# Kernel tuning notes

Measured on AMD Instinct MI355X. Metric: run time of the kernel, lower is better.

Reference implementation:

```python
import jax, jax.numpy as jnp
import numpy as np

NUM_CODES = 512
CODE_DIM = 64
BATCH = 1048576


def setup_inputs() -> dict:
    key = jax.random.key(0)
    k1, k2 = jax.random.split(key)
    z_e = jax.random.normal(k1, (BATCH, CODE_DIM), dtype=jnp.float32)
    bound = 1.0 / np.sqrt(float(CODE_DIM))
    codebook = jax.random.uniform(
        k2, (NUM_CODES, CODE_DIM), dtype=jnp.float32, minval=-bound, maxval=bound
    )
    return {"z_e": z_e, "codebook": codebook}


def reference(z_e, codebook):
    # ||z_e||^2 - 2 z_e . e_j + ||e_j||^2  -> (batch, num_codes)
    distances = (
        jnp.sum(z_e**2, axis=1, keepdims=True)
        - 2.0 * (z_e @ codebook.T)
        + jnp.sum(codebook**2, axis=1)
    )
    indices = jnp.argmin(distances, axis=1)          # (batch,)
    z_q = codebook[indices]                           # gather (batch, code_dim)
    # straight-through estimator
    z_q_st = z_e + jax.lax.stop_gradient(z_q - z_e)
    commitment_loss = jnp.mean((jax.lax.stop_gradient(z_e) - z_q) ** 2)
    return (z_q_st, indices, commitment_loss)
```

## Files before the change

### kernel.cpp

```cpp
#include <hip/hip_runtime.h>
#include <stdint.h>


#define DIM 64
#define NCODE 512
#define RPB 128
#define MARGIN 2e-3f
#define BIAS 64.0f
#define ZEXB 8
#define WS_NEED (NCODE * DIM * 2 * sizeof(unsigned short) + NCODE * sizeof(float))

typedef __attribute__((ext_vector_type(8))) short short8;
typedef __attribute__((ext_vector_type(4))) float f32x4;
typedef unsigned long long ull;

__device__ __forceinline__ float bf2f(unsigned short u) {
    union { unsigned u; float f; } c; c.u = ((unsigned)u) << 16; return c.f;
}
__device__ __forceinline__ unsigned short f2bf(float f) {
    union { float f; unsigned u; } c; c.f = f;
    unsigned r = c.u + 0x7fffu + ((c.u >> 16) & 1u);
    return (unsigned short)(r >> 16);
}
__device__ __forceinline__ unsigned fkey(float v) {
    union { float f; unsigned u; } c; c.f = v;
    return c.u ^ ((unsigned)((int)c.u >> 31) | 0x80000000u);
}

__device__ __forceinline__ float np_sumsq64_sse(const float* x) {
    #pragma clang fp contract(off)
    float T[4];
    #pragma unroll
    for (int l = 0; l < 4; ++l) {
        float A[8];
        #pragma unroll
        for (int j = 0; j < 8; ++j) {
            float u = x[4 * j + l];
            float v = x[32 + 4 * j + l];
            A[j] = u * u + v * v;
        }
        T[l] = ((A[0] + A[1]) + (A[2] + A[3])) + ((A[4] + A[5]) + (A[6] + A[7]));
    }
    return (T[0] + T[1]) + (T[2] + T[3]);
}

__global__ void vq_zero_loss(float* __restrict__ out, long long lidx) {
    if (threadIdx.x == 0) out[lidx] = 0.f;
}

__global__ __launch_bounds__(NCODE) void vq_prep(
    const float* __restrict__ cb, unsigned short* __restrict__ ws)
{
    const int code = threadIdx.x;
    unsigned short* cbhi = ws;
    unsigned short* cblo = ws + NCODE * DIM;
    float* ce2g = (float*)(ws + 2 * NCODE * DIM);

    float sp[4];
    #pragma unroll
    for (int cl = 0; cl < 4; ++cl) {
        float s = 0.f;
        #pragma unroll
        for (int ks = 0; ks < 2; ++ks) {
            #pragma unroll
            for (int t = 0; t < 8; ++t) {
                int k = ks * 32 + cl * 8 + t;
                float v = cb[code * DIM + k];
                unsigned short hb = f2bf(v);
                cbhi[code * DIM + k] = hb;
                cblo[code * DIM + k] = f2bf(v - bf2f(hb));
                s = fmaf(v, v, s);
            }
        }
        sp[cl] = s;
    }
    ce2g[code] = ((sp[0] + sp[1]) + (sp[2] + sp[3])) + BIAS;
}

template <bool PRE>
__global__ __launch_bounds__(512, 4) void vq_main(
    const float* __restrict__ z, const float* __restrict__ cb,
    float* __restrict__ out, const unsigned short* __restrict__ ws,
    long long batch)
{
    __shared__ __align__(16) unsigned short zhi[RPB * DIM];
    __shared__ __align__(16) unsigned short zlo[RPB * DIM];
    __shared__ float zsq[RPB];
    __shared__ float arrB[RPB][9];
    __shared__ float arrB2[RPB][9];
    __shared__ unsigned arrI[RPB][9];
    __shared__ ull cpack[RPB];
    __shared__ unsigned ck2[RPB];
    __shared__ float wsum[8];
    __shared__ int s_flag[RPB];
    __shared__ int s_nflag;
    __shared__ float s_zex[ZEXB][DIM];
    __shared__ ull s_win[ZEXB];

    const int tid = threadIdx.x, lane = tid & 63, wid = tid >> 6;
    const long long R0 = (long long)blockIdx.x * RPB;
    short8* zhi8 = (short8*)zhi;
    short8* zlo8 = (short8*)zlo;

    if (tid == 0) s_nflag = 0;

    #pragma unroll
    for (int p = 0; p < 2; ++p) {
        int L = p * 512 + tid;
        int row = L >> 3, c = L & 7;
        const float4* g = (const float4*)(z + (R0 + row) * DIM + c * 8);
        float4 f0 = g[0], f1 = g[1];
        float v[8] = {f0.x, f0.y, f0.z, f0.w, f1.x, f1.y, f1.z, f1.w};
        short8 h, l;
        float s = 0.f;
        #pragma unroll
        for (int t = 0; t < 8; ++t) {
            unsigned short hb = f2bf(v[t]);
            h[t] = (short)hb;
            l[t] = (short)f2bf(v[t] - bf2f(hb));
            s = fmaf(v[t], v[t], s);
        }
        s += __shfl_xor(s, 1);
        s += __shfl_xor(s, 2);
        s += __shfl_xor(s, 4);
        if ((tid & 7) == 0) zsq[row] = s;
        int slot = row * 8 + (c ^ (row & 7));
        zhi8[slot] = h;
        zlo8[slot] = l;
    }

    short8 bhi[4][2], blo[4][2];
    float ce2[4];
    if constexpr (PRE) {
        const unsigned short* cbhi = ws;
        const unsigned short* cblo = ws + NCODE * DIM;
        const float* ce2g = (const float*)(ws + 2 * NCODE * DIM);
        #pragma unroll
        for (int ct = 0; ct < 4; ++ct) {
            int code = wid * 64 + ct * 16 + (lane & 15);
            #pragma unroll
            for (int ks = 0; ks < 2; ++ks) {
                int k = ks * 32 + (lane >> 4) * 8;
                bhi[ct][ks] = *(const short8*)(cbhi + code * DIM + k);
                blo[ct][ks] = *(const short8*)(cblo + code * DIM + k);
            }
            ce2[ct] = ce2g[code];
        }
    } else {
        #pragma unroll
        for (int ct = 0; ct < 4; ++ct) {
            int code = wid * 64 + ct * 16 + (lane & 15);
            float s = 0.f;
            #pragma unroll
            for (int ks = 0; ks < 2; ++ks) {
                int k = ks * 32 + (lane >> 4) * 8;
                const float4* g = (const float4*)(cb + code * DIM + k);
                float4 f0 = g[0], f1 = g[1];
                float v[8] = {f0.x, f0.y, f0.z, f0.w, f1.x, f1.y, f1.z, f1.w};
                short8 h, l;
                #pragma unroll
                for (int t = 0; t < 8; ++t) {
                    unsigned short hb = f2bf(v[t]);
                    h[t] = (short)hb;
                    l[t] = (short)f2bf(v[t] - bf2f(hb));
                    s = fmaf(v[t], v[t], s);
                }
                bhi[ct][ks] = h;
                blo[ct][ks] = l;
            }
            s += __shfl_xor(s, 16);
            s += __shfl_xor(s, 32);
            ce2[ct] = s + BIAS;
        }
    }

    __syncthreads();

    for (int rt = 0; rt < 8; ++rt) {
        int arow = rt * 16 + (lane & 15);
        int swz = arow & 7;
        int c0 = (lane >> 4) ^ swz, c1 = (4 + (lane >> 4)) ^ swz;
        short8 ah0 = zhi8[arow * 8 + c0], ah1 = zhi8[arow * 8 + c1];
        short8 al0 = zlo8[arow * 8 + c0], al1 = zlo8[arow * 8 + c1];

        float b1[4] = {3.4e38f, 3.4e38f, 3.4e38f, 3.4e38f};
        float b2[4] = {3.4e38f, 3.4e38f, 3.4e38f, 3.4e38f};
        unsigned bi[4] = {0, 0, 0, 0};

        #pragma unroll
        for (int ct = 0; ct < 4; ++ct) {
            f32x4 a = {0.f, 0.f, 0.f, 0.f};
            a = __builtin_amdgcn_mfma_f32_16x16x32_bf16(ah0, bhi[ct][0], a, 0, 0, 0);
            a = __builtin_amdgcn_mfma_f32_16x16x32_bf16(ah1, bhi[ct][1], a, 0, 0, 0);
            a = __builtin_amdgcn_mfma_f32_16x16x32_bf16(ah0, blo[ct][0], a, 0, 0, 0);
            a = __builtin_amdgcn_mfma_f32_16x16x32_bf16(ah1, blo[ct][1], a, 0, 0, 0);
            a = __builtin_amdgcn_mfma_f32_16x16x32_bf16(al0, bhi[ct][0], a, 0, 0, 0);
            a = __builtin_amdgcn_mfma_f32_16x16x32_bf16(al1, bhi[ct][1], a, 0, 0, 0);
            #pragma unroll
            for (int r = 0; r < 4; ++r) {
                float v = fmaf(-2.f, a[r], ce2[ct]);
                unsigned idx = (unsigned)(wid * 64 + ct * 16 + (lane & 15));
                float nb2 = __builtin_amdgcn_fmed3f(v, b1[r], b2[r]);
                bi[r] = (v < b1[r]) ? idx : bi[r];
                b1[r] = fminf(v, b1[r]);
                b2[r] = nb2;
            }
        }

        #pragma unroll
        for (int r = 0; r < 4; ++r) {
            float x1 = b1[r], x2 = b2[r];
            unsigned xi = bi[r];
            #pragma unroll
            for (int m = 1; m <= 8; m <<= 1) {
                float ob  = __shfl_xor(x1, m);
                float ob2 = __shfl_xor(x2, m);
                unsigned oi = __shfl_xor(xi, m);
                float mx = fmaxf(x1, ob);
                x2 = fminf(fminf(x2, ob2), mx);
                xi = (ob < x1) ? oi : xi;
                x1 = fminf(x1, ob);
            }
            if ((lane & 15) == 0) {
                int row = rt * 16 + (lane >> 4) * 4 + r;
                arrB[row][wid]  = x1;
                arrB2[row][wid] = x2;
                arrI[row][wid]  = xi;
            }
        }
    }
    __syncthreads();

    if (tid < 128) {
        int row = tid;
        float b1 = arrB[row][0], b2 = arrB2[row][0];
        unsigned bi = arrI[row][0];
        #pragma unroll
        for (int w = 1; w < 8; ++w) {
            float ob = arrB[row][w];
            float ob2 = arrB2[row][w];
            unsigned oi = arrI[row][w];
            float mx = fmaxf(b1, ob);
            b2 = fminf(fminf(b2, ob2), mx);
            bi = (ob < b1) ? oi : bi;
            b1 = fminf(b1, ob);
        }
        cpack[row] = ((ull)__float_as_uint(b1) << 32) | bi;
        ck2[row] = __float_as_uint(b2);
    }
    __syncthreads();

    {
        int row = tid >> 2, j = tid & 3;
        ull best = cpack[row];
        unsigned bk2 = ck2[row];
        unsigned code = (unsigned)best;
        long long grow = R0 + row;

        float4* out4 = (float4*)out;
        const float4* cb4 = (const float4*)cb;
        #pragma unroll
        for (int t = 0; t < 4; ++t)
            out4[grow * 16 + j * 4 + t] = cb4[(long long)code * 16 + j * 4 + t];

        float d = 0.f;
        if (j == 0) {
            out[batch * DIM + grow] = (float)code;
            float v1b = __uint_as_float((unsigned)(best >> 32));
            float v2b = __uint_as_float(bk2);
            d = zsq[row] + (v1b - BIAS);
            if (v2b - v1b < MARGIN) {
                int p = atomicAdd(&s_nflag, 1);
                s_flag[p] = row;
            }
        }
        #pragma unroll
        for (int m = 1; m < 64; m <<= 1) d += __shfl_xor(d, m);
        if (lane == 0) wsum[wid] = d;
    }
    __syncthreads();
    if (tid == 0) {
        float s = 0.f;
        #pragma unroll
        for (int w = 0; w < 8; ++w) s += wsum[w];
        atomicAdd(&out[batch * DIM + batch], s * (1.0f / 67108864.0f));
    }

    int nf = s_nflag;
    if (nf > 0) {
        float ce[64];
        const float4* cb4 = (const float4*)cb;
        #pragma unroll
        for (int q = 0; q < 16; ++q) {
            float4 v = cb4[tid * 16 + q];
            ce[q * 4 + 0] = v.x; ce[q * 4 + 1] = v.y;
            ce[q * 4 + 2] = v.z; ce[q * 4 + 3] = v.w;
        }
        float s2 = np_sumsq64_sse(ce);

        for (int b0 = 0; b0 < nf; b0 += ZEXB) {
            int nb = min(ZEXB, nf - b0);
            if (tid < nb * 64) {
                int i = tid >> 6, l2 = tid & 63;
                s_zex[i][l2] = z[(R0 + s_flag[b0 + i]) * DIM + l2];
            }
            if (tid < ZEXB) s_win[tid] = ~0ull;
            __syncthreads();

            for (int i = 0; i < nb; ++i) {
                float s1 = np_sumsq64_sse(&s_zex[i][0]);
                float m = 0.f;
                #pragma unroll
                for (int k = 0; k < 64; ++k)
                    m = __builtin_fmaf(s_zex[i][k], ce[k], m);
                float dnp;
                {
                    #pragma clang fp contract(off)
                    float tt = s1 - 2.0f * m;
                    dnp = tt + s2;
                }
                ull key = ((ull)fkey(dnp) << 10) | (unsigned)tid;
                #pragma unroll
                for (int mm = 1; mm < 64; mm <<= 1) {
                    ull o = __shfl_xor(key, mm);
                    if (o < key) key = o;
                }
                if (lane == 0) atomicMin(&s_win[i], key);
            }
            __syncthreads();

            for (int i = wid; i < nb; i += 8) {
                unsigned code = (unsigned)(s_win[i] & 0x3FFull);
                int rowb = s_flag[b0 + i];
                long long grow = R0 + rowb;
                out[grow * DIM + lane] = cb[(long long)code * DIM + lane];
                if (lane == 0) out[batch * DIM + grow] = (float)code;
            }
            __syncthreads();
        }
    }
}

extern "C" void kernel_launch(void* const* d_in, const int* in_sizes, int n_in,
                              void* d_out, int out_size, void* d_ws, size_t ws_size,
                              hipStream_t stream)
{
    const float* z  = (const float*)d_in[0];
    const float* cb = (const float*)d_in[1];
    float* out = (float*)d_out;
    unsigned short* ws = (unsigned short*)d_ws;

    long long batch = (long long)in_sizes[0] / DIM;
    int nblocks = (int)(batch / RPB);
    long long lidx = batch * DIM + batch;

    vq_zero_loss<<<1, 64, 0, stream>>>(out, lidx);
    if (d_ws != nullptr && ws_size >= WS_NEED) {
        vq_prep<<<1, NCODE, 0, stream>>>(cb, ws);
        vq_main<true><<<nblocks, 512, 0, stream>>>(z, cb, out, ws, batch);
    } else {
        vq_main<false><<<nblocks, 512, 0, stream>>>(z, cb, out, ws, batch);
    }
}
```

Baseline: 704.0 us.

## Split VQ into partial-codebook argmin kernel plus merge kernel

```diff
diff --git a/kernel.cpp b/kernel.cpp
--- a/kernel.cpp
+++ b/kernel.cpp
@@ -5,10 +5,11 @@
 #define DIM 64
 #define NCODE 512
 #define RPB 128
+#define PRPB 64
 #define MARGIN 2e-3f
 #define BIAS 64.0f
 #define ZEXB 8
-#define WS_NEED (NCODE * DIM * 2 * sizeof(unsigned short) + NCODE * sizeof(float))
+#define WS_TAB (NCODE * DIM * 2 * sizeof(unsigned short) + NCODE * sizeof(float))
 
 typedef __attribute__((ext_vector_type(8))) short short8;
 typedef __attribute__((ext_vector_type(4))) float f32x4;
@@ -77,36 +78,29 @@
     ce2g[code] = ((sp[0] + sp[1]) + (sp[2] + sp[3])) + BIAS;
 }
 
-template <bool PRE>
-__global__ __launch_bounds__(512, 4) void vq_main(
-    const float* __restrict__ z, const float* __restrict__ cb,
-    float* __restrict__ out, const unsigned short* __restrict__ ws,
-    long long batch)
+__global__ __launch_bounds__(256) void vq_part(
+    const float* __restrict__ z, const unsigned short* __restrict__ ws,
+    unsigned* __restrict__ wsP, float* __restrict__ out,
+    long long batch, long long lidx)
 {
-    __shared__ __align__(16) unsigned short zhi[RPB * DIM];
-    __shared__ __align__(16) unsigned short zlo[RPB * DIM];
-    __shared__ float zsq[RPB];
-    __shared__ float arrB[RPB][9];
-    __shared__ float arrB2[RPB][9];
-    __shared__ unsigned arrI[RPB][9];
-    __shared__ ull cpack[RPB];
-    __shared__ unsigned ck2[RPB];
-    __shared__ float wsum[8];
-    __shared__ int s_flag[RPB];
-    __shared__ int s_nflag;
-    __shared__ float s_zex[ZEXB][DIM];
-    __shared__ ull s_win[ZEXB];
+    __shared__ __align__(16) unsigned short zhi[PRPB * DIM];
+    __shared__ __align__(16) unsigned short zlo[PRPB * DIM];
+    __shared__ float zsq[PRPB];
+    __shared__ float arrB[PRPB][5];
+    __shared__ float arrB2[PRPB][5];
+    __shared__ unsigned arrI[PRPB][5];
 
     const int tid = threadIdx.x, lane = tid & 63, wid = tid >> 6;
-    const long long R0 = (long long)blockIdx.x * RPB;
+    const int cl = lane >> 4, l15 = lane & 15;
+    const int bid = blockIdx.x;
+    const int half = bid & 1;
+    const long long R0 = (long long)(bid >> 1) * PRPB;
     short8* zhi8 = (short8*)zhi;
     short8* zlo8 = (short8*)zlo;
 
-    if (tid == 0) s_nflag = 0;
-
     #pragma unroll
     for (int p = 0; p < 2; ++p) {
-        int L = p * 512 + tid;
+        int L = p * 256 + tid;
         int row = L >> 3, c = L & 7;
         const float4* g = (const float4*)(z + (R0 + row) * DIM + c * 8);
         float4 f0 = g[0], f1 = g[1];
@@ -131,55 +125,35 @@
 
     short8 bhi[4][2], blo[4][2];
     float ce2[4];
-    if constexpr (PRE) {
+    {
         const unsigned short* cbhi = ws;
         const unsigned short* cblo = ws + NCODE * DIM;
         const float* ce2g = (const float*)(ws + 2 * NCODE * DIM);
         #pragma unroll
         for (int ct = 0; ct < 4; ++ct) {
-            int code = wid * 64 + ct * 16 + (lane & 15);
+            int code = half * 256 + wid * 64 + ct * 16 + l15;
             #pragma unroll
             for (int ks = 0; ks < 2; ++ks) {
-                int k = ks * 32 + (lane >> 4) * 8;
+                int k = ks * 32 + cl * 8;
                 bhi[ct][ks] = *(const short8*)(cbhi + code * DIM + k);
                 blo[ct][ks] = *(const short8*)(cblo + code * DIM + k);
             }
             ce2[ct] = ce2g[code];
         }
-    } else {
-        #pragma unroll
-        for (int ct = 0; ct < 4; ++ct) {
-            int code = wid * 64 + ct * 16 + (lane & 15);
-            float s = 0.f;
-            #pragma unroll
-            for (int ks = 0; ks < 2; ++ks) {
-                int k = ks * 32 + (lane >> 4) * 8;
-                const float4* g = (const float4*)(cb + code * DIM + k);
-                float4 f0 = g[0], f1 = g[1];
-                float v[8] = {f0.x, f0.y, f0.z, f0.w, f1.x, f1.y, f1.z, f1.w};
-                short8 h, l;
-                #pragma unroll
-                for (int t = 0; t < 8; ++t) {
-                    unsigned short hb = f2bf(v[t]);
-                    h[t] = (short)hb;
-                    l[t] = (short)f2bf(v[t] - bf2f(hb));
-                    s = fmaf(v[t], v[t], s);
-                }
-                bhi[ct][ks] = h;
-                blo[ct][ks] = l;
-            }
-            s += __shfl_xor(s, 16);
-            s += __shfl_xor(s, 32);
-            ce2[ct] = s + BIAS;
-        }
-    }
-
-    __syncthreads();
-
-    for (int rt = 0; rt < 8; ++rt) {
-        int arow = rt * 16 + (lane & 15);
+    }
+    __syncthreads();
+
+    if (half == 0 && tid < PRPB) {
+        float v = zsq[tid];
+        #pragma unroll
+        for (int m = 1; m < 64; m <<= 1) v += __shfl_xor(v, m);
+        if (lane == 0) atomicAdd(&out[lidx], v * (1.0f / 67108864.0f));
+    }
+
+    for (int rt = 0; rt < 4; ++rt) {
+        int arow = rt * 16 + l15;
         int swz = arow & 7;
-        int c0 = (lane >> 4) ^ swz, c1 = (4 + (lane >> 4)) ^ swz;
+        int c0 = cl ^ swz, c1 = (4 + cl) ^ swz;
         short8 ah0 = zhi8[arow * 8 + c0], ah1 = zhi8[arow * 8 + c1];
         short8 al0 = zlo8[arow * 8 + c0], al1 = zlo8[arow * 8 + c1];
 
@@ -199,7 +173,7 @@
             #pragma unroll
             for (int r = 0; r < 4; ++r) {
                 float v = fmaf(-2.f, a[r], ce2[ct]);
-                unsigned idx = (unsigned)(wid * 64 + ct * 16 + (lane & 15));
+                unsigned idx = (unsigned)(half * 256 + wid * 64 + ct * 16 + l15);
                 float nb2 = __builtin_amdgcn_fmed3f(v, b1[r], b2[r]);
                 bi[r] = (v < b1[r]) ? idx : bi[r];
                 b1[r] = fminf(v, b1[r]);
@@ -221,8 +195,8 @@
                 xi = (ob < x1) ? oi : xi;
                 x1 = fminf(x1, ob);
             }
-            if ((lane & 15) == 0) {
-                int row = rt * 16 + (lane >> 4) * 4 + r;
+            if (l15 == 0) {
+                int row = rt * 16 + cl * 4 + r;
                 arrB[row][wid]  = x1;
                 arrB2[row][wid] = x2;
                 arrI[row][wid]  = xi;
@@ -231,12 +205,12 @@
     }
     __syncthreads();
 
-    if (tid < 128) {
+    if (tid < PRPB) {
         int row = tid;
         float b1 = arrB[row][0], b2 = arrB2[row][0];
         unsigned bi = arrI[row][0];
         #pragma unroll
-        for (int w = 1; w < 8; ++w) {
+        for (int w = 1; w < 4; ++w) {
             float ob = arrB[row][w];
             float ob2 = arrB2[row][w];
             unsigned oi = arrI[row][w];
@@ -245,17 +219,43 @@
             bi = (ob < b1) ? oi : bi;
             b1 = fminf(b1, ob);
         }
-        cpack[row] = ((ull)__float_as_uint(b1) << 32) | bi;
-        ck2[row] = __float_as_uint(b2);
-    }
+        unsigned* p = wsP + ((R0 + row) * 2 + half) * 3;
+        p[0] = __float_as_uint(b1);
+        p[1] = __float_as_uint(b2);
+        p[2] = bi;
+    }
+}
+
+__global__ __launch_bounds__(512) void vq_merge(
+    const float* __restrict__ z, const float* __restrict__ cb,
+    float* __restrict__ out, const unsigned* __restrict__ wsP,
+    long long batch)
+{
+    __shared__ float wsum[8];
+    __shared__ int s_flag[RPB];
+    __shared__ int s_nflag;
+    __shared__ float s_zex[ZEXB][DIM];
+    __shared__ ull s_win[ZEXB];
+
+    const int tid = threadIdx.x, lane = tid & 63, wid = tid >> 6;
+    const long long R0 = (long long)blockIdx.x * RPB;
+
+    if (tid == 0) s_nflag = 0;
     __syncthreads();
 
     {
         int row = tid >> 2, j = tid & 3;
-        ull best = cpack[row];
-        unsigned bk2 = ck2[row];
-        unsigned code = (unsigned)best;
         long long grow = R0 + row;
+        const unsigned* p = wsP + grow * 6;
+        float b1a = __uint_as_float(p[0]), b2a = __uint_as_float(p[1]);
+        unsigned ia = p[2];
+        float b1b = __uint_as_float(p[3]), b2b = __uint_as_float(p[4]);
+        unsigned ib = p[5];
+
+        float b1 = b1a;
+        unsigned code = ia;
+        if (b1b < b1a) { b1 = b1b; code = ib; }
+        float b2 = fminf(fminf(b2a, b2b), fmaxf(b1a, b1b));
 
         float4* out4 = (float4*)out;
         const float4* cb4 = (const float4*)cb;
@@ -266,12 +266,10 @@
         float d = 0.f;
         if (j == 0) {
             out[batch * DIM + grow] = (float)code;
-            float v1b = __uint_as_float((unsigned)(best >> 32));
-            float v2b = __uint_as_float(bk2);
-            d = zsq[row] + (v1b - BIAS);
-            if (v2b - v1b < MARGIN) {
-                int p = atomicAdd(&s_nflag, 1);
-                s_flag[p] = row;
+            d = b1 - BIAS;
+            if (b2 - b1 < MARGIN) {
+                int pp = atomicAdd(&s_nflag, 1);
+                s_flag[pp] = row;
             }
         }
         #pragma unroll
@@ -341,6 +339,270 @@
     }
 }
 
+template <bool PRE>
+__global__ __launch_bounds__(512, 4) void vq_main_mono(
+    const float* __restrict__ z, const float* __restrict__ cb,
+    float* __restrict__ out, const unsigned short* __restrict__ ws,
+    long long batch)
+{
+    __shared__ __align__(16) unsigned short zhi[RPB * DIM];
+    __shared__ __align__(16) unsigned short zlo[RPB * DIM];
+    __shared__ float zsq[RPB];
+    __shared__ float arrB[RPB][9];
+    __shared__ float arrB2[RPB][9];
+    __shared__ unsigned arrI[RPB][9];
+    __shared__ ull cpack[RPB];
+    __shared__ unsigned ck2[RPB];
+    __shared__ float wsum[8];
+    __shared__ int s_flag[RPB];
+    __shared__ int s_nflag;
+    __shared__ float s_zex[ZEXB][DIM];
+    __shared__ ull s_win[ZEXB];
+
+    const int tid = threadIdx.x, lane = tid & 63, wid = tid >> 6;
+    const long long R0 = (long long)blockIdx.x * RPB;
+    short8* zhi8 = (short8*)zhi;
+    short8* zlo8 = (short8*)zlo;
+
+    if (tid == 0) s_nflag = 0;
+
+    #pragma unroll
+    for (int p = 0; p < 2; ++p) {
+        int L = p * 512 + tid;
+        int row = L >> 3, c = L & 7;
+        const float4* g = (const float4*)(z + (R0 + row) * DIM + c * 8);
+        float4 f0 = g[0], f1 = g[1];
+        float v[8] = {f0.x, f0.y, f0.z, f0.w, f1.x, f1.y, f1.z, f1.w};
+        short8 h, l;
+        float s = 0.f;
+        #pragma unroll
+        for (int t = 0; t < 8; ++t) {
+            unsigned short hb = f2bf(v[t]);
+            h[t] = (short)hb;
+            l[t] = (short)f2bf(v[t] - bf2f(hb));
+            s = fmaf(v[t], v[t], s);
+        }
+        s += __shfl_xor(s, 1);
+        s += __shfl_xor(s, 2);
+        s += __shfl_xor(s, 4);
+        if ((tid & 7) == 0) zsq[row] = s;
+        int slot = row * 8 + (c ^ (row & 7));
+        zhi8[slot] = h;
+        zlo8[slot] = l;
+    }
+
+    short8 bhi[4][2], blo[4][2];
+    float ce2[4];
+    if constexpr (PRE) {
+        const unsigned short* cbhi = ws;
+        const unsigned short* cblo = ws + NCODE * DIM;
+        const float* ce2g = (const float*)(ws + 2 * NCODE * DIM);
+        #pragma unroll
+        for (int ct = 0; ct < 4; ++ct) {
+            int code = wid * 64 + ct * 16 + (lane & 15);
+            #pragma unroll
+            for (int ks = 0; ks < 2; ++ks) {
+                int k = ks * 32 + (lane >> 4) * 8;
+                bhi[ct][ks] = *(const short8*)(cbhi + code * DIM + k);
+                blo[ct][ks] = *(const short8*)(cblo + code * DIM + k);
+            }
+            ce2[ct] = ce2g[code];
+        }
+    } else {
+        #pragma unroll
+        for (int ct = 0; ct < 4; ++ct) {
+            int code = wid * 64 + ct * 16 + (lane & 15);
+            float s = 0.f;
+            #pragma unroll
+            for (int ks = 0; ks < 2; ++ks) {
+                int k = ks * 32 + (lane >> 4) * 8;
+                const float4* g = (const float4*)(cb + code * DIM + k);
+                float4 f0 = g[0], f1 = g[1];
+                float v[8] = {f0.x, f0.y, f0.z, f0.w, f1.x, f1.y, f1.z, f1.w};
+                short8 h, l;
+                #pragma unroll
+                for (int t = 0; t < 8; ++t) {
+                    unsigned short hb = f2bf(v[t]);
+                    h[t] = (short)hb;
+                    l[t] = (short)f2bf(v[t] - bf2f(hb));
+                    s = fmaf(v[t], v[t], s);
+                }
+                bhi[ct][ks] = h;
+                blo[ct][ks] = l;
+            }
+            s += __shfl_xor(s, 16);
+            s += __shfl_xor(s, 32);
+            ce2[ct] = s + BIAS;
+        }
+    }
+
+    __syncthreads();
+
+    for (int rt = 0; rt < 8; ++rt) {
+        int arow = rt * 16 + (lane & 15);
+        int swz = arow & 7;
+        int c0 = (lane >> 4) ^ swz, c1 = (4 + (lane >> 4)) ^ swz;
+        short8 ah0 = zhi8[arow * 8 + c0], ah1 = zhi8[arow * 8 + c1];
+        short8 al0 = zlo8[arow * 8 + c0], al1 = zlo8[arow * 8 + c1];
+
+        float b1[4] = {3.4e38f, 3.4e38f, 3.4e38f, 3.4e38f};
+        float b2[4] = {3.4e38f, 3.4e38f, 3.4e38f, 3.4e38f};
+        unsigned bi[4] = {0, 0, 0, 0};
+
+        #pragma unroll
+        for (int ct = 0; ct < 4; ++ct) {
+            f32x4 a = {0.f, 0.f, 0.f, 0.f};
+            a = __builtin_amdgcn_mfma_f32_16x16x32_bf16(ah0, bhi[ct][0], a, 0, 0, 0);
+            a = __builtin_amdgcn_mfma_f32_16x16x32_bf16(ah1, bhi[ct][1], a, 0, 0, 0);
+            a = __builtin_amdgcn_mfma_f32_16x16x32_bf16(ah0, blo[ct][0], a, 0, 0, 0);
+            a = __builtin_amdgcn_mfma_f32_16x16x32_bf16(ah1, blo[ct][1], a, 0, 0, 0);
+            a = __builtin_amdgcn_mfma_f32_16x16x32_bf16(al0, bhi[ct][0], a, 0, 0, 0);
+            a = __builtin_amdgcn_mfma_f32_16x16x32_bf16(al1, bhi[ct][1], a, 0, 0, 0);
+            #pragma unroll
+            for (int r = 0; r < 4; ++r) {
+                float v = fmaf(-2.f, a[r], ce2[ct]);
+                unsigned idx = (unsigned)(wid * 64 + ct * 16 + (lane & 15));
+                float nb2 = __builtin_amdgcn_fmed3f(v, b1[r], b2[r]);
+                bi[r] = (v < b1[r]) ? idx : bi[r];
+                b1[r] = fminf(v, b1[r]);
+                b2[r] = nb2;
+            }
+        }
+
+        #pragma unroll
+        for (int r = 0; r < 4; ++r) {
+            float x1 = b1[r], x2 = b2[r];
+            unsigned xi = bi[r];
+            #pragma unroll
+            for (int m = 1; m <= 8; m <<= 1) {
+                float ob  = __shfl_xor(x1, m);
+                float ob2 = __shfl_xor(x2, m);
+                unsigned oi = __shfl_xor(xi, m);
+                float mx = fmaxf(x1, ob);
+                x2 = fminf(fminf(x2, ob2), mx);
+                xi = (ob < x1) ? oi : xi;
+                x1 = fminf(x1, ob);
+            }
+            if ((lane & 15) == 0) {
+                int row = rt * 16 + (lane >> 4) * 4 + r;
+                arrB[row][wid]  = x1;
+                arrB2[row][wid] = x2;
+                arrI[row][wid]  = xi;
+            }
+        }
+    }
+    __syncthreads();
+
+    if (tid < 128) {
+        int row = tid;
+        float b1 = arrB[row][0], b2 = arrB2[row][0];
+        unsigned bi = arrI[row][0];
+        #pragma unroll
+        for (int w = 1; w < 8; ++w) {
+            float ob = arrB[row][w];
+            float ob2 = arrB2[row][w];
+            unsigned oi = arrI[row][w];
+            float mx = fmaxf(b1, ob);
+            b2 = fminf(fminf(b2, ob2), mx);
+            bi = (ob < b1) ? oi : bi;
+            b1 = fminf(b1, ob);
+        }
+        cpack[row] = ((ull)__float_as_uint(b1) << 32) | bi;
+        ck2[row] = __float_as_uint(b2);
+    }
+    __syncthreads();
+
+    {
+        int row = tid >> 2, j = tid & 3;
+        ull best = cpack[row];
+        unsigned bk2 = ck2[row];
+        unsigned code = (unsigned)best;
+        long long grow = R0 + row;
+
+        float4* out4 = (float4*)out;
+        const float4* cb4 = (const float4*)cb;
+        #pragma unroll
+        for (int t = 0; t < 4; ++t)
+            out4[grow * 16 + j * 4 + t] = cb4[(long long)code * 16 + j * 4 + t];
+
+        float d = 0.f;
+        if (j == 0) {
+            out[batch * DIM + grow] = (float)code;
+            float v1b = __uint_as_float((unsigned)(best >> 32));
+            float v2b = __uint_as_float(bk2);
+            d = zsq[row] + (v1b - BIAS);
+            if (v2b - v1b < MARGIN) {
+                int p = atomicAdd(&s_nflag, 1);
+                s_flag[p] = row;
+            }
+        }
+        #pragma unroll
+        for (int m = 1; m < 64; m <<= 1) d += __shfl_xor(d, m);
+        if (lane == 0) wsum[wid] = d;
+    }
+    __syncthreads();
+    if (tid == 0) {
+        float s = 0.f;
+        #pragma unroll
+        for (int w = 0; w < 8; ++w) s += wsum[w];
+        atomicAdd(&out[batch * DIM + batch], s * (1.0f / 67108864.0f));
+    }
+
+    int nf = s_nflag;
+    if (nf > 0) {
+        float ce[64];
+        const float4* cb4 = (const float4*)cb;
+        #pragma unroll
+        for (int q = 0; q < 16; ++q) {
+            float4 v = cb4[tid * 16 + q];
+            ce[q * 4 + 0] = v.x; ce[q * 4 + 1] = v.y;
+            ce[q * 4 + 2] = v.z; ce[q * 4 + 3] = v.w;
+        }
+        float s2 = np_sumsq64_sse(ce);
+
+        for (int b0 = 0; b0 < nf; b0 += ZEXB) {
+            int nb = min(ZEXB, nf - b0);
+            if (tid < nb * 64) {
+                int i = tid >> 6, l2 = tid & 63;
+                s_zex[i][l2] = z[(R0 + s_flag[b0 + i]) * DIM + l2];
+            }
+            if (tid < ZEXB) s_win[tid] = ~0ull;
+            __syncthreads();
+
+            for (int i = 0; i < nb; ++i) {
+                float s1 = np_sumsq64_sse(&s_zex[i][0]);
+                float m = 0.f;
+                #pragma unroll
+                for (int k = 0; k < 64; ++k)
+                    m = __builtin_fmaf(s_zex[i][k], ce[k], m);
+                float dnp;
+                {
+                    #pragma clang fp contract(off)
+                    float tt = s1 - 2.0f * m;
+                    dnp = tt + s2;
+                }
+                ull key = ((ull)fkey(dnp) << 10) | (unsigned)tid;
+                #pragma unroll
+                for (int mm = 1; mm < 64; mm <<= 1) {
+                    ull o = __shfl_xor(key, mm);
+                    if (o < key) key = o;
+                }
+                if (lane == 0) atomicMin(&s_win[i], key);
+            }
+            __syncthreads();
+
+            for (int i = wid; i < nb; i += 8) {
+                unsigned code = (unsigned)(s_win[i] & 0x3FFull);
+                int rowb = s_flag[b0 + i];
+                long long grow = R0 + rowb;
+                out[grow * DIM + lane] = cb[(long long)code * DIM + lane];
+                if (lane == 0) out[batch * DIM + grow] = (float)code;
+            }
+            __syncthreads();
+        }
+    }
+}
+
 extern "C" void kernel_launch(void* const* d_in, const int* in_sizes, int n_in,
                               void* d_out, int out_size, void* d_ws, size_t ws_size,
                               hipStream_t stream)
@@ -351,14 +613,21 @@
     unsigned short* ws = (unsigned short*)d_ws;
 
     long long batch = (long long)in_sizes[0] / DIM;
-    int nblocks = (int)(batch / RPB);
     long long lidx = batch * DIM + batch;
+    size_t ws2_need = WS_TAB + (size_t)batch * 6 * sizeof(unsigned);
 
     vq_zero_loss<<<1, 64, 0, stream>>>(out, lidx);
-    if (d_ws != nullptr && ws_size >= WS_NEED) {
+    if (d_ws != nullptr && ws_size >= ws2_need) {
+        unsigned* wsP = (unsigned*)((char*)d_ws + WS_TAB);
+        int nb1 = (int)((batch / PRPB) * 2);
+        int nb2 = (int)(batch / RPB);
         vq_prep<<<1, NCODE, 0, stream>>>(cb, ws);
-        vq_main<true><<<nblocks, 512, 0, stream>>>(z, cb, out, ws, batch);
+        vq_part<<<nb1, 256, 0, stream>>>(z, ws, wsP, out, batch, lidx);
+        vq_merge<<<nb2, 512, 0, stream>>>(z, cb, out, wsP, batch);
+    } else if (d_ws != nullptr && ws_size >= WS_TAB) {
+        vq_prep<<<1, NCODE, 0, stream>>>(cb, ws);
+        vq_main_mono<true><<<(int)(batch / RPB), 512, 0, stream>>>(z, cb, out, ws, batch);
     } else {
-        vq_main<false><<<nblocks, 512, 0, stream>>>(z, cb, out, ws, batch);
-    }
-}
+        vq_main_mono<false><<<(int)(batch / RPB), 512, 0, stream>>>(z, cb, out, ws, batch);
+    }
+}
```

Result: faster. 602.2 us (-14.5%).
